# Kernel optimization log

Measured on AMD Instinct MI355X. Metric: run time of the kernel, lower is better.

Reference implementation:

```python
import jax, jax.numpy as jnp
import numpy as np

H, W, R = 512, 512, 4
H8, W8 = H // 8, W // 8  # 64, 64
B, C = 4, 256


def _offsets(r):
    # diamond window: y in [-r, r], x in [|y|-r, r-|y|]  ->  2r^2+2r+1 offsets
    offs = []
    for y in range(-r, r + 1):
        for x in range(abs(y) - r, r - abs(y) + 1):
            offs.append((y, x))
    return np.asarray(offs, dtype=np.float32)  # [L, 2] = (dy, dx)

_OFFS = _offsets(R)  # L = 41


def _corr_pyramid(f1, f2):
    # over the second image's spatial dims for each pyramid level.
    c = jnp.einsum('bcij,bcuv->bijuv', f1, f2) / jnp.sqrt(jnp.float32(f1.shape[1]))
    pyr = [c]
    for _ in range(3):
        b, i, j, h, w = pyr[-1].shape
        pyr.append(pyr[-1].reshape(b, i, j, h // 2, 2, w // 2, 2).mean(axis=(4, 6)))
    return pyr  # shapes [B,64,64,64/2^k,64/2^k] for k=0..3


def _bilinear_zeros(volf, py, px, h, w):
    # volf: [B,H8,W8,h*w]; py/px: [B,H8,W8,L] pixel coords; zero padding.
    y0 = jnp.floor(py); x0 = jnp.floor(px)
    wy1 = py - y0; wy0 = 1.0 - wy1
    wx1 = px - x0; wx0 = 1.0 - wx1

    def gather(yi, xi):
        valid = (yi >= 0) & (yi < h) & (xi >= 0) & (xi < w)
        yc = jnp.clip(yi, 0, h - 1).astype(jnp.int32)
        xc = jnp.clip(xi, 0, w - 1).astype(jnp.int32)
        v = jnp.take_along_axis(volf, yc * w + xc, axis=-1)
        return jnp.where(valid, v, jnp.zeros((), volf.dtype))

    return (wy0 * wx0 * gather(y0, x0) + wy0 * wx1 * gather(y0, x0 + 1)
            + wy1 * wx0 * gather(y0 + 1, x0) + wy1 * wx1 * gather(y0 + 1, x0 + 1))


def _lookup_level(corr, flow, k):
    # corr: [B,H8,W8,h,w]; flow: [B,2,H8,W8] (chan 0 = dy, chan 1 = dx)
    b, _, _, h, w = corr.shape
    dy = jnp.asarray(_OFFS[:, 0]); dx = jnp.asarray(_OFFS[:, 1])
    ii = jnp.arange(H8, dtype=corr.dtype)[:, None]   # [H8,1]
    jj = jnp.arange(W8, dtype=corr.dtype)[None, :]   # [1,W8]
    scale = jnp.float32(2.0 ** k)
    yc = (ii[None] + flow[:, 0]) / scale             # [B,H8,W8]
    xc = (jj[None] + flow[:, 1]) / scale
    py = yc[..., None] + dy                          # [B,H8,W8,L]
    px = xc[..., None] + dx
    # original normalizes by dim/2 (not (dim-1)/2), grid_sample align_corners=True
    # maps normalized g -> pixel (g+1)*(dim-1)/2, net: pixel = coord*(dim-1)/dim
    py = py * (h - 1) / h
    px = px * (w - 1) / w
    volf = corr.reshape(b, H8, W8, h * w)
    return _bilinear_zeros(volf, py, px, h, w)       # [B,H8,W8,L]


def setup_inputs() -> dict:
    key = jax.random.key(0)
    k1, k2, k3 = jax.random.split(key, 3)
    feat1 = jax.random.normal(k1, (B, C, H8, W8), dtype=jnp.float32)
    feat2 = jax.random.normal(k2, (B, C, H8, W8), dtype=jnp.float32)
    curr_flow = jax.random.normal(k3, (B, 2, H8, W8), dtype=jnp.float32)
    return {"feat1": feat1, "feat2": feat2, "curr_flow": curr_flow}


def reference(feat1, feat2, curr_flow):
    pyr = _corr_pyramid(feat1, feat2)
    lookups = [_lookup_level(pyr[k], curr_flow, k) for k in range(4)]
    return jnp.stack(lookups, axis=3)  # [B, H8, W8, 4, 41]
```

## Files before the change

### kernel.cpp

```cpp
#include <hip/hip_runtime.h>
#include <stdint.h>

#define NB 4
#define NC 256
#define FB   1392640
#define LVO1 1048576
#define LVO2 1310720
#define LVO3 1376256

typedef short bf16x8 __attribute__((ext_vector_type(8)));
typedef float f32x4  __attribute__((ext_vector_type(4)));

__device__ __forceinline__ unsigned short f2b(float x){
  uint32_t u = __float_as_uint(x);
  return (unsigned short)((u + 0x7FFFu + ((u >> 16) & 1u)) >> 16);
}
__device__ __forceinline__ unsigned int pack2(float a, float b){
  return (unsigned int)f2b(a) | ((unsigned int)f2b(b) << 16);
}

__global__ __launch_bounds__(256) void prep_all(const float* __restrict__ f1,
                 const float* __restrict__ f2,
                 unsigned short* __restrict__ f1t,
                 unsigned short* __restrict__ f2c){
  __shared__ float lds[128*65];
  __shared__ float l1s[32*65];
  __shared__ float l2s[8*65];
  const int t = threadIdx.x;
  const int bx = blockIdx.x;

  if (bx < 2048){
    const int b = bx >> 9, rest = bx & 511;
    const int cc = rest >> 7, pt = rest & 127;
    const int p0 = pt*32, c0 = cc*64;
    const int tx = t & 31, ty = t >> 5;
    float (*tileF)[33] = (float(*)[33])lds;
    #pragma unroll
    for (int r = 0; r < 8; ++r){
      int c = ty + r*8;
      tileF[c][tx] = f1[((size_t)(b*NC) + c0 + c)*4096 + p0 + tx];
    }
    __syncthreads();
    #pragma unroll
    for (int r = 0; r < 4; ++r){
      int pl = ty + r*8;
      size_t o = ((size_t)(b*4096 + p0 + pl))*NC;
      *(unsigned int*)(f1t + o + c0 + 2*tx) = pack2(tileF[2*tx][pl], tileF[2*tx+1][pl]);
    }
  } else {
    const int fid = bx - 2048;
    const int b = fid >> 7, rest = fid & 127;
    const int reg = rest >> 2, cc = rest & 3;
    const int i0 = (reg >> 2) * 8, j0 = (reg & 3) * 16;
    const int c0 = cc * 64, qb = cc * 8;

    #pragma unroll
    for (int it = 0; it < 8; ++it){
      int q = t + 256*it;
      int ch = q >> 5, rc = q & 31, ri = rc >> 2, c4 = rc & 3;
      const float4 v = *(const float4*)(f2 + ((size_t)(b*NC) + c0 + ch)*4096
                                          + (i0+ri)*64 + j0 + c4*4);
      float* dstL = lds + (ri*16 + c4*4)*65 + ch;
      dstL[0] = v.x; dstL[65] = v.y; dstL[130] = v.z; dstL[195] = v.w;
    }
    __syncthreads();
    unsigned short* f2cB = f2c + (size_t)b*FB;

    #pragma unroll
    for (int it = 0; it < 4; ++it){
      int idx = t + 256*it;
      int cell = idx & 127, qi = idx >> 7;
      int ci = cell >> 4, cj = cell & 15;
      const float* src = lds + cell*65 + qi*8;
      uint4 v;
      v.x = pack2(src[0], src[1]); v.y = pack2(src[2], src[3]);
      v.z = pack2(src[4], src[5]); v.w = pack2(src[6], src[7]);
      int cellg = (i0+ci)*64 + j0+cj;
      *(uint4*)(f2cB + ((size_t)(qb+qi)*4096 + cellg)*8) = v;
    }
    {
      int cell = t & 31, qi = t >> 5;
      int a = cell >> 3, bc = cell & 7;
      const float* p00 = lds + ((2*a)*16 + 2*bc)*65 + qi*8;
      float s[8];
      #pragma unroll
      for (int j = 0; j < 8; ++j){
        s[j] = p00[j] + p00[65+j] + p00[16*65+j] + p00[17*65+j];
        l1s[cell*65 + qi*8 + j] = s[j];
      }
      uint4 v;
      v.x = pack2(s[0]*0.25f, s[1]*0.25f); v.y = pack2(s[2]*0.25f, s[3]*0.25f);
      v.z = pack2(s[4]*0.25f, s[5]*0.25f); v.w = pack2(s[6]*0.25f, s[7]*0.25f);
      int cellg = ((i0>>1)+a)*32 + (j0>>1)+bc;
      *(uint4*)(f2cB + LVO1 + ((size_t)(qb+qi)*1024 + cellg)*8) = v;
    }
    __syncthreads();
    if (t < 64){
      int cell = t & 7, qi = t >> 3;
      int a2 = cell >> 2, bc2 = cell & 3;
      float s[8];
      #pragma unroll
      for (int j = 0; j < 8; ++j){
        int ch = qi*8 + j;
        s[j] = l1s[((2*a2)*8   + 2*bc2  )*65 + ch] + l1s[((2*a2)*8   + 2*bc2+1)*65 + ch]
             + l1s[((2*a2+1)*8 + 2*bc2  )*65 + ch] + l1s[((2*a2+1)*8 + 2*bc2+1)*65 + ch];
        l2s[cell*65 + ch] = s[j];
      }
      uint4 v;
      v.x = pack2(s[0]*0.0625f, s[1]*0.0625f); v.y = pack2(s[2]*0.0625f, s[3]*0.0625f);
      v.z = pack2(s[4]*0.0625f, s[5]*0.0625f); v.w = pack2(s[6]*0.0625f, s[7]*0.0625f);
      int cellg = ((i0>>2)+a2)*16 + (j0>>2)+bc2;
      *(uint4*)(f2cB + LVO2 + ((size_t)(qb+qi)*256 + cellg)*8) = v;
    }
    __syncthreads();
    if (t < 16){
      int cl = t & 1, qi = t >> 1;
      float s[8];
      #pragma unroll
      for (int j = 0; j < 8; ++j){
        int ch = qi*8 + j;
        s[j] = l2s[(0*4 + 2*cl)*65 + ch] + l2s[(0*4 + 2*cl+1)*65 + ch]
             + l2s[(1*4 + 2*cl)*65 + ch] + l2s[(1*4 + 2*cl+1)*65 + ch];
      }
      const float m = 1.0f/64.0f;
      uint4 v;
      v.x = pack2(s[0]*m, s[1]*m); v.y = pack2(s[2]*m, s[3]*m);
      v.z = pack2(s[4]*m, s[5]*m); v.w = pack2(s[6]*m, s[7]*m);
      int cellg = (i0>>3)*8 + (j0>>3) + cl;
      *(uint4*)(f2cB + LVO3 + ((size_t)(qb+qi)*64 + cellg)*8) = v;
    }
  }
}

__global__ __launch_bounds__(256, 4) void lookup_main(const float* __restrict__ flow,
                 const unsigned short* __restrict__ f1t,
                 const unsigned short* __restrict__ f2c,
                 float* __restrict__ out){
  const int lane = threadIdx.x & 63;
  const int wid  = threadIdx.x >> 6;
  const int blk = blockIdx.x;
  const int xs = blk & 7;
  const int bb = xs >> 1;
  const int tile = ((blk >> 3) << 1) | (xs & 1);
  const int ti4 = (tile >> 4) << 2;
  const int tj4 = (tile & 15) << 2;

  __shared__ float box[4*16*113];
  __shared__ int   ls_y0[64], ls_x0[64];
  __shared__ float ls_f[32];
  __shared__ int   ls_meta[32];

  {
    float4* b4 = (float4*)box;
    for (int q = threadIdx.x; q < (4*16*113)/4; q += 256)
      b4[q] = make_float4(0.f, 0.f, 0.f, 0.f);
  }

  const int n = lane & 15;
  const int g = lane >> 4;
  const int pn = ((ti4 + (n >> 2)) << 6) + tj4 + (n & 3);

  bf16x8 bfr[8];
  {
    const unsigned short* f1c = f1t + ((size_t)(bb*4096 + pn))*NC;
    #pragma unroll
    for (int st = 0; st < 8; ++st)
      bfr[st] = *(const bf16x8*)(f1c + st*32 + g*8);
  }

  if (wid == 0){
    const int k = g;
    const int i_n = pn >> 6, j_n = pn & 63;
    const float fy = flow[((bb*2 + 0)*64 + i_n)*64 + j_n];
    const float fx = flow[((bb*2 + 1)*64 + i_n)*64 + j_n];
    if (k == 0){ ls_f[n] = fy; ls_f[16 + n] = fx; }
    const int h = 64 >> k;
    const float inv = 1.0f / (float)(1 << k);
    const float s = (float)(h - 1) / (float)h;
    const float yc = ((float)i_n + fy) * inv;
    const float xc = ((float)j_n + fx) * inv;
    const int y0 = (int)floorf((yc - 4.0f) * s);
    const int x0 = (int)floorf((xc - 4.0f) * s);
    ls_y0[k*16 + n] = y0;
    ls_x0[k*16 + n] = x0;
    int ymin = y0, ymax = y0, xmin = x0, xmax = x0;
    #pragma unroll
    for (int m = 1; m < 16; m <<= 1){
      ymin = min(ymin, __shfl_xor(ymin, m));
      ymax = max(ymax, __shfl_xor(ymax, m));
      xmin = min(xmin, __shfl_xor(xmin, m));
      xmax = max(xmax, __shfl_xor(xmax, m));
    }
    if (n == 0){
      int ylo = max(ymin, 0), yhi = min(ymax + 9, h - 1);
      int xlo = max(xmin, 0), xhi = min(xmax + 9, h - 1);
      int H = max(yhi - ylo + 1, 0), W = max(xhi - xlo + 1, 0);
      int cells = W * H;
      ls_meta[k*8 + 0] = ylo;
      ls_meta[k*8 + 1] = xlo;
      ls_meta[k*8 + 2] = W;
      ls_meta[k*8 + 3] = cells;
      ls_meta[k*8 + 4] = __float_as_int(1.0f / (float)W);
      ls_meta[k*8 + 5] = (k==0) ? 0 : (k==1) ? LVO1 : (k==2) ? LVO2 : LVO3;
      ls_meta[k*8 + 6] = (cells + 15) >> 4;
    }
  }
  __syncthreads();

  const int y0n0 = ls_y0[n],      x0n0 = ls_x0[n];
  const int y0n1 = ls_y0[16 + n], x0n1 = ls_x0[16 + n];
  const int y0n2 = ls_y0[32 + n], x0n2 = ls_x0[32 + n];
  const int y0n3 = ls_y0[48 + n], x0n3 = ls_x0[48 + n];
  const int pre1 = ls_meta[6];
  const int pre2 = pre1 + ls_meta[14];
  const int pre3 = pre2 + ls_meta[22];
  const int P    = pre3 + ls_meta[30];
  const unsigned short* f2cB = f2c + (size_t)bb*FB;

  for (int p = wid; p < P; p += 4){
    const int k  = (p >= pre1) + (p >= pre2) + (p >= pre3);
    const int lp = p - ((k==0) ? 0 : (k==1) ? pre1 : (k==2) ? pre2 : pre3);
    const int mb = k*8;
    const int ylo = ls_meta[mb], xlo = ls_meta[mb+1], W = ls_meta[mb+2];
    const int cells = ls_meta[mb+3];
    const float rW = __int_as_float(ls_meta[mb+4]);
    const int lvoc = ls_meta[mb+5];
    const int h = 64 >> k;
    const int ncl = h*h;
    const int base = lp << 4;

    const int idxA = min(base + n, cells - 1);
    const int by = (int)fmaf((float)idxA, rW, 0.004f);
    const int bx = idxA - by*W;
    const int cellIdx = (ylo + by)*h + (xlo + bx);
    const unsigned short* colp = f2cB + lvoc + ((size_t)(g*ncl + cellIdx) << 3);
    const int strideS = ncl << 5;

    f32x4 acc0 = {0.f,0.f,0.f,0.f}, acc1 = {0.f,0.f,0.f,0.f};
    #pragma unroll
    for (int st = 0; st < 8; st += 2){
      bf16x8 a0 = *(const bf16x8*)(colp + (size_t)st*strideS);
      bf16x8 a1 = *(const bf16x8*)(colp + (size_t)(st+1)*strideS);
      acc0 = __builtin_amdgcn_mfma_f32_16x16x32_bf16(a0, bfr[st],   acc0, 0, 0, 0);
      acc1 = __builtin_amdgcn_mfma_f32_16x16x32_bf16(a1, bfr[st+1], acc1, 0, 0, 0);
    }
    const int yb = (k==0) ? y0n0 : (k==1) ? y0n1 : (k==2) ? y0n2 : y0n3;
    const int xb = (k==0) ? x0n0 : (k==1) ? x0n1 : (k==2) ? x0n2 : x0n3;
    #pragma unroll
    for (int r = 0; r < 4; ++r){
      const int ci = base + (g << 2) + r;
      if (ci < cells){
        const int byc = (int)fmaf((float)ci, rW, 0.004f);
        const int bxc = ci - byc*W;
        const int ry = ylo + byc - yb;
        const int rx = xlo + bxc - xb;
        if ((unsigned)ry < 10u && (unsigned)rx < 10u)
          box[(k*16 + n)*113 + ry*10 + rx] = (acc0[r] + acc1[r]) * 0.0625f;
      }
    }
  }
  __syncthreads();

  int dy = 0, dx = 0;
  {
    int rem = lane;
    #pragma unroll
    for (int ry = -4; ry <= 4; ++ry){
      int ab = ry < 0 ? -ry : ry;
      int ln = 9 - 2*ab;
      if (rem >= 0 && rem < ln){ dy = ry; dx = rem + (ab - 4); }
      rem -= ln;
    }
  }
  const int k = wid;
  const float inv = 1.0f / (float)(1 << k);
  const float s = (float)((64 >> k) - 1) / (float)(64 >> k);
  if (lane < 41){
    for (int t = 0; t < 16; ++t){
      const int pt = ((ti4 + (t >> 2)) << 6) + tj4 + (t & 3);
      const float fy = ls_f[t], fx = ls_f[16 + t];
      const float yc = ((float)(pt >> 6) + fy) * inv;
      const float xc = ((float)(pt & 63) + fx) * inv;
      const float py = (yc + (float)dy) * s;
      const float px = (xc + (float)dx) * s;
      const float fy0 = floorf(py), fx0 = floorf(px);
      const float wy1 = py - fy0, wx1 = px - fx0;
      const float wy0 = 1.0f - wy1, wx0 = 1.0f - wx1;
      const int iy = (int)fy0 - ls_y0[k*16 + t];
      const int ix = (int)fx0 - ls_x0[k*16 + t];
      const float* bx_ = &box[(k*16 + t)*113 + iy*10 + ix];
      const float v = wy0*(wx0*bx_[0] + wx1*bx_[1]) + wy1*(wx0*bx_[10] + wx1*bx_[11]);
      out[((size_t)(bb*4096 + pt)*4 + k)*41 + lane] = v;
    }
  }
}

extern "C" void kernel_launch(void* const* d_in, const int* in_sizes, int n_in,
                              void* d_out, int out_size, void* d_ws, size_t ws_size,
                              hipStream_t stream){
  const float* feat1 = (const float*)d_in[0];
  const float* feat2 = (const float*)d_in[1];
  const float* flow  = (const float*)d_in[2];
  float* out = (float*)d_out;
  unsigned short* f1t = (unsigned short*)d_ws;
  unsigned short* f2c = f1t + (size_t)NB*4096*NC;

  prep_all<<<2560, 256, 0, stream>>>(feat1, feat2, f1t, f2c);
  lookup_main<<<1024, 256, 0, stream>>>(flow, f1t, f2c, out);
}
```

Before: 111.2 us.

## Software-pipeline A-fragment loads in lookup loop and widen feat1 transpose tiles

The lookup loop now prefetches the next work item's eight bf16 A fragments and metadata before running the MFMAs on the current item, so global-load latency overlaps with compute. Separately, the feat1 transpose in the prep kernel uses 64x64 tiles with float4 loads and 16-byte packed bf16 stores, which halves that part of the grid. Double-buffered fragments raise register pressure under launch_bounds(256,4), and the wider tile may bring more LDS bank conflicts on the strided reads.

```diff
diff --git a/kernel.cpp b/kernel.cpp
--- a/kernel.cpp
+++ b/kernel.cpp
@@ -29,26 +29,33 @@
   const int t = threadIdx.x;
   const int bx = blockIdx.x;
 
-  if (bx < 2048){
-    const int b = bx >> 9, rest = bx & 511;
-    const int cc = rest >> 7, pt = rest & 127;
-    const int p0 = pt*32, c0 = cc*64;
-    const int tx = t & 31, ty = t >> 5;
-    float (*tileF)[33] = (float(*)[33])lds;
-    #pragma unroll
-    for (int r = 0; r < 8; ++r){
-      int c = ty + r*8;
-      tileF[c][tx] = f1[((size_t)(b*NC) + c0 + c)*4096 + p0 + tx];
+  if (bx < 1024){
+    const int b = bx >> 8;
+    const int rest = bx & 255;
+    const int pt = rest >> 2, cc = rest & 3;
+    const int p0 = pt*64, c0 = cc*64;
+    #pragma unroll
+    for (int it = 0; it < 4; ++it){
+      int idx = t + 256*it;
+      int row = idx >> 4, c4 = idx & 15;
+      const float4 v = *(const float4*)(f1 + ((size_t)(b*NC) + c0 + row)*4096
+                                          + p0 + c4*4);
+      float* d = lds + row*65 + c4*4;
+      d[0]=v.x; d[1]=v.y; d[2]=v.z; d[3]=v.w;
     }
     __syncthreads();
     #pragma unroll
-    for (int r = 0; r < 4; ++r){
-      int pl = ty + r*8;
-      size_t o = ((size_t)(b*4096 + p0 + pl))*NC;
-      *(unsigned int*)(f1t + o + c0 + 2*tx) = pack2(tileF[2*tx][pl], tileF[2*tx+1][pl]);
+    for (int it = 0; it < 2; ++it){
+      int idx = t + 256*it;
+      int px = idx >> 3, ch8 = idx & 7;
+      const float* s = lds + (ch8*8)*65 + px;
+      uint4 v;
+      v.x = pack2(s[0],   s[65]);  v.y = pack2(s[130], s[195]);
+      v.z = pack2(s[260], s[325]); v.w = pack2(s[390], s[455]);
+      *(uint4*)(f1t + ((size_t)(b*4096 + p0 + px))*NC + c0 + ch8*8) = v;
     }
   } else {
-    const int fid = bx - 2048;
+    const int fid = bx - 1024;
     const int b = fid >> 7, rest = fid & 127;
     const int reg = rest >> 2, cc = rest & 3;
     const int i0 = (reg >> 2) * 8, j0 = (reg & 3) * 16;
@@ -131,6 +138,12 @@
     }
   }
 }
+
+struct PM {
+  const unsigned short* colp;
+  int strideS, k, base, ylo, xlo, W, cells, yb, xb;
+  float rW;
+};
 
 __global__ __launch_bounds__(256, 4) void lookup_main(const float* __restrict__ flow,
                  const unsigned short* __restrict__ f1t,
@@ -217,47 +230,70 @@
   const int P    = pre3 + ls_meta[30];
   const unsigned short* f2cB = f2c + (size_t)bb*FB;
 
-  for (int p = wid; p < P; p += 4){
-    const int k  = (p >= pre1) + (p >= pre2) + (p >= pre3);
-    const int lp = p - ((k==0) ? 0 : (k==1) ? pre1 : (k==2) ? pre2 : pre3);
-    const int mb = k*8;
-    const int ylo = ls_meta[mb], xlo = ls_meta[mb+1], W = ls_meta[mb+2];
-    const int cells = ls_meta[mb+3];
-    const float rW = __int_as_float(ls_meta[mb+4]);
+  auto mk = [&](int p)->PM{
+    PM m;
+    m.k = (p >= pre1) + (p >= pre2) + (p >= pre3);
+    const int lp = p - ((m.k==0) ? 0 : (m.k==1) ? pre1 : (m.k==2) ? pre2 : pre3);
+    const int mb = m.k*8;
+    m.ylo = ls_meta[mb]; m.xlo = ls_meta[mb+1]; m.W = ls_meta[mb+2];
+    m.cells = ls_meta[mb+3]; m.rW = __int_as_float(ls_meta[mb+4]);
     const int lvoc = ls_meta[mb+5];
-    const int h = 64 >> k;
-    const int ncl = h*h;
-    const int base = lp << 4;
-
-    const int idxA = min(base + n, cells - 1);
-    const int by = (int)fmaf((float)idxA, rW, 0.004f);
-    const int bx = idxA - by*W;
-    const int cellIdx = (ylo + by)*h + (xlo + bx);
-    const unsigned short* colp = f2cB + lvoc + ((size_t)(g*ncl + cellIdx) << 3);
-    const int strideS = ncl << 5;
-
+    const int h = 64 >> m.k, ncl = h*h;
+    m.base = lp << 4;
+    const int idxA = min(m.base + n, m.cells - 1);
+    const int by = (int)fmaf((float)idxA, m.rW, 0.004f);
+    const int bx = idxA - by*m.W;
+    m.colp = f2cB + lvoc + ((size_t)(g*ncl + (m.ylo + by)*h + (m.xlo + bx)) << 3);
+    m.strideS = ncl << 5;
+    m.yb = (m.k==0) ? y0n0 : (m.k==1) ? y0n1 : (m.k==2) ? y0n2 : y0n3;
+    m.xb = (m.k==0) ? x0n0 : (m.k==1) ? x0n1 : (m.k==2) ? x0n2 : x0n3;
+    return m;
+  };
+
+  bf16x8 afr[8];
+  PM cur;
+  int p = wid;
+  if (p < P){
+    cur = mk(p);
+    #pragma unroll
+    for (int st = 0; st < 8; ++st)
+      afr[st] = *(const bf16x8*)(cur.colp + (size_t)st*cur.strideS);
+  }
+  while (p < P){
+    const int np = p + 4;
+    PM nxt;
+    bf16x8 nfr[8];
+    const bool has = np < P;
+    if (has){
+      nxt = mk(np);
+      #pragma unroll
+      for (int st = 0; st < 8; ++st)
+        nfr[st] = *(const bf16x8*)(nxt.colp + (size_t)st*nxt.strideS);
+    }
     f32x4 acc0 = {0.f,0.f,0.f,0.f}, acc1 = {0.f,0.f,0.f,0.f};
     #pragma unroll
     for (int st = 0; st < 8; st += 2){
-      bf16x8 a0 = *(const bf16x8*)(colp + (size_t)st*strideS);
-      bf16x8 a1 = *(const bf16x8*)(colp + (size_t)(st+1)*strideS);
-      acc0 = __builtin_amdgcn_mfma_f32_16x16x32_bf16(a0, bfr[st],   acc0, 0, 0, 0);
-      acc1 = __builtin_amdgcn_mfma_f32_16x16x32_bf16(a1, bfr[st+1], acc1, 0, 0, 0);
-    }
-    const int yb = (k==0) ? y0n0 : (k==1) ? y0n1 : (k==2) ? y0n2 : y0n3;
-    const int xb = (k==0) ? x0n0 : (k==1) ? x0n1 : (k==2) ? x0n2 : x0n3;
+      acc0 = __builtin_amdgcn_mfma_f32_16x16x32_bf16(afr[st],   bfr[st],   acc0, 0, 0, 0);
+      acc1 = __builtin_amdgcn_mfma_f32_16x16x32_bf16(afr[st+1], bfr[st+1], acc1, 0, 0, 0);
+    }
     #pragma unroll
     for (int r = 0; r < 4; ++r){
-      const int ci = base + (g << 2) + r;
-      if (ci < cells){
-        const int byc = (int)fmaf((float)ci, rW, 0.004f);
-        const int bxc = ci - byc*W;
-        const int ry = ylo + byc - yb;
-        const int rx = xlo + bxc - xb;
+      const int ci = cur.base + (g << 2) + r;
+      if (ci < cur.cells){
+        const int byc = (int)fmaf((float)ci, cur.rW, 0.004f);
+        const int bxc = ci - byc*cur.W;
+        const int ry = cur.ylo + byc - cur.yb;
+        const int rx = cur.xlo + bxc - cur.xb;
         if ((unsigned)ry < 10u && (unsigned)rx < 10u)
-          box[(k*16 + n)*113 + ry*10 + rx] = (acc0[r] + acc1[r]) * 0.0625f;
+          box[(cur.k*16 + n)*113 + ry*10 + rx] = (acc0[r] + acc1[r]) * 0.0625f;
       }
     }
+    if (has){
+      cur = nxt;
+      #pragma unroll
+      for (int st = 0; st < 8; ++st) afr[st] = nfr[st];
+    }
+    p = np;
   }
   __syncthreads();
 
@@ -305,6 +341,6 @@
   unsigned short* f1t = (unsigned short*)d_ws;
   unsigned short* f2c = f1t + (size_t)NB*4096*NC;
 
-  prep_all<<<2560, 256, 0, stream>>>(feat1, feat2, f1t, f2c);
+  prep_all<<<1536, 256, 0, stream>>>(feat1, feat2, f1t, f2c);
   lookup_main<<<1024, 256, 0, stream>>>(flow, f1t, f2c, out);
 }
```

Measured after the change: 127.0 us. 1.14x slower.

## Fuse feat1 transpose and bf16 conversion into lookup kernel via LDS

Applied to the files above, without the earlier changes.

Removes the feat1 transpose/convert blocks from the prep kernel. The lookup kernel now loads its 16 query pixels' fp32 feat1 channels directly, converts them to bf16 into a padded LDS tile, and reads the MFMA B fragments from LDS. This drops the f1t workspace round-trip (write, then read) and cuts the prep grid from 2560 to 512 blocks. In exchange it adds about 8 KB of LDS per block and strided global reads of feat1 inside lookup_main, which may lower occupancy.

```diff
diff --git a/kernel.cpp b/kernel.cpp
--- a/kernel.cpp
+++ b/kernel.cpp
@@ -19,121 +19,97 @@
   return (unsigned int)f2b(a) | ((unsigned int)f2b(b) << 16);
 }
 
-__global__ __launch_bounds__(256) void prep_all(const float* __restrict__ f1,
-                 const float* __restrict__ f2,
-                 unsigned short* __restrict__ f1t,
+__global__ __launch_bounds__(256) void prep_all(const float* __restrict__ f2,
                  unsigned short* __restrict__ f2c){
   __shared__ float lds[128*65];
   __shared__ float l1s[32*65];
   __shared__ float l2s[8*65];
   const int t = threadIdx.x;
-  const int bx = blockIdx.x;
-
-  if (bx < 2048){
-    const int b = bx >> 9, rest = bx & 511;
-    const int cc = rest >> 7, pt = rest & 127;
-    const int p0 = pt*32, c0 = cc*64;
-    const int tx = t & 31, ty = t >> 5;
-    float (*tileF)[33] = (float(*)[33])lds;
-    #pragma unroll
-    for (int r = 0; r < 8; ++r){
-      int c = ty + r*8;
-      tileF[c][tx] = f1[((size_t)(b*NC) + c0 + c)*4096 + p0 + tx];
-    }
-    __syncthreads();
-    #pragma unroll
-    for (int r = 0; r < 4; ++r){
-      int pl = ty + r*8;
-      size_t o = ((size_t)(b*4096 + p0 + pl))*NC;
-      *(unsigned int*)(f1t + o + c0 + 2*tx) = pack2(tileF[2*tx][pl], tileF[2*tx+1][pl]);
-    }
-  } else {
-    const int fid = bx - 2048;
-    const int b = fid >> 7, rest = fid & 127;
-    const int reg = rest >> 2, cc = rest & 3;
-    const int i0 = (reg >> 2) * 8, j0 = (reg & 3) * 16;
-    const int c0 = cc * 64, qb = cc * 8;
-
-    #pragma unroll
-    for (int it = 0; it < 8; ++it){
-      int q = t + 256*it;
-      int ch = q >> 5, rc = q & 31, ri = rc >> 2, c4 = rc & 3;
-      const float4 v = *(const float4*)(f2 + ((size_t)(b*NC) + c0 + ch)*4096
-                                          + (i0+ri)*64 + j0 + c4*4);
-      float* dstL = lds + (ri*16 + c4*4)*65 + ch;
-      dstL[0] = v.x; dstL[65] = v.y; dstL[130] = v.z; dstL[195] = v.w;
-    }
-    __syncthreads();
-    unsigned short* f2cB = f2c + (size_t)b*FB;
-
-    #pragma unroll
-    for (int it = 0; it < 4; ++it){
-      int idx = t + 256*it;
-      int cell = idx & 127, qi = idx >> 7;
-      int ci = cell >> 4, cj = cell & 15;
-      const float* src = lds + cell*65 + qi*8;
-      uint4 v;
-      v.x = pack2(src[0], src[1]); v.y = pack2(src[2], src[3]);
-      v.z = pack2(src[4], src[5]); v.w = pack2(src[6], src[7]);
-      int cellg = (i0+ci)*64 + j0+cj;
-      *(uint4*)(f2cB + ((size_t)(qb+qi)*4096 + cellg)*8) = v;
-    }
-    {
-      int cell = t & 31, qi = t >> 5;
-      int a = cell >> 3, bc = cell & 7;
-      const float* p00 = lds + ((2*a)*16 + 2*bc)*65 + qi*8;
-      float s[8];
-      #pragma unroll
-      for (int j = 0; j < 8; ++j){
-        s[j] = p00[j] + p00[65+j] + p00[16*65+j] + p00[17*65+j];
-        l1s[cell*65 + qi*8 + j] = s[j];
-      }
-      uint4 v;
-      v.x = pack2(s[0]*0.25f, s[1]*0.25f); v.y = pack2(s[2]*0.25f, s[3]*0.25f);
-      v.z = pack2(s[4]*0.25f, s[5]*0.25f); v.w = pack2(s[6]*0.25f, s[7]*0.25f);
-      int cellg = ((i0>>1)+a)*32 + (j0>>1)+bc;
-      *(uint4*)(f2cB + LVO1 + ((size_t)(qb+qi)*1024 + cellg)*8) = v;
-    }
-    __syncthreads();
-    if (t < 64){
-      int cell = t & 7, qi = t >> 3;
-      int a2 = cell >> 2, bc2 = cell & 3;
-      float s[8];
-      #pragma unroll
-      for (int j = 0; j < 8; ++j){
-        int ch = qi*8 + j;
-        s[j] = l1s[((2*a2)*8   + 2*bc2  )*65 + ch] + l1s[((2*a2)*8   + 2*bc2+1)*65 + ch]
-             + l1s[((2*a2+1)*8 + 2*bc2  )*65 + ch] + l1s[((2*a2+1)*8 + 2*bc2+1)*65 + ch];
-        l2s[cell*65 + ch] = s[j];
-      }
-      uint4 v;
-      v.x = pack2(s[0]*0.0625f, s[1]*0.0625f); v.y = pack2(s[2]*0.0625f, s[3]*0.0625f);
-      v.z = pack2(s[4]*0.0625f, s[5]*0.0625f); v.w = pack2(s[6]*0.0625f, s[7]*0.0625f);
-      int cellg = ((i0>>2)+a2)*16 + (j0>>2)+bc2;
-      *(uint4*)(f2cB + LVO2 + ((size_t)(qb+qi)*256 + cellg)*8) = v;
-    }
-    __syncthreads();
-    if (t < 16){
-      int cl = t & 1, qi = t >> 1;
-      float s[8];
-      #pragma unroll
-      for (int j = 0; j < 8; ++j){
-        int ch = qi*8 + j;
-        s[j] = l2s[(0*4 + 2*cl)*65 + ch] + l2s[(0*4 + 2*cl+1)*65 + ch]
-             + l2s[(1*4 + 2*cl)*65 + ch] + l2s[(1*4 + 2*cl+1)*65 + ch];
-      }
-      const float m = 1.0f/64.0f;
-      uint4 v;
-      v.x = pack2(s[0]*m, s[1]*m); v.y = pack2(s[2]*m, s[3]*m);
-      v.z = pack2(s[4]*m, s[5]*m); v.w = pack2(s[6]*m, s[7]*m);
-      int cellg = (i0>>3)*8 + (j0>>3) + cl;
-      *(uint4*)(f2cB + LVO3 + ((size_t)(qb+qi)*64 + cellg)*8) = v;
-    }
+  const int fid = blockIdx.x;
+  const int b = fid >> 7, rest = fid & 127;
+  const int reg = rest >> 2, cc = rest & 3;
+  const int i0 = (reg >> 2) * 8, j0 = (reg & 3) * 16;
+  const int c0 = cc * 64, qb = cc * 8;
+
+  #pragma unroll
+  for (int it = 0; it < 8; ++it){
+    int q = t + 256*it;
+    int ch = q >> 5, rc = q & 31, ri = rc >> 2, c4 = rc & 3;
+    const float4 v = *(const float4*)(f2 + ((size_t)(b*NC) + c0 + ch)*4096
+                                        + (i0+ri)*64 + j0 + c4*4);
+    float* dstL = lds + (ri*16 + c4*4)*65 + ch;
+    dstL[0] = v.x; dstL[65] = v.y; dstL[130] = v.z; dstL[195] = v.w;
+  }
+  __syncthreads();
+  unsigned short* f2cB = f2c + (size_t)b*FB;
+
+  #pragma unroll
+  for (int it = 0; it < 4; ++it){
+    int idx = t + 256*it;
+    int cell = idx & 127, qi = idx >> 7;
+    int ci = cell >> 4, cj = cell & 15;
+    const float* src = lds + cell*65 + qi*8;
+    uint4 v;
+    v.x = pack2(src[0], src[1]); v.y = pack2(src[2], src[3]);
+    v.z = pack2(src[4], src[5]); v.w = pack2(src[6], src[7]);
+    int cellg = (i0+ci)*64 + j0+cj;
+    *(uint4*)(f2cB + ((size_t)(qb+qi)*4096 + cellg)*8) = v;
+  }
+  {
+    int cell = t & 31, qi = t >> 5;
+    int a = cell >> 3, bc = cell & 7;
+    const float* p00 = lds + ((2*a)*16 + 2*bc)*65 + qi*8;
+    float s[8];
+    #pragma unroll
+    for (int j = 0; j < 8; ++j){
+      s[j] = p00[j] + p00[65+j] + p00[16*65+j] + p00[17*65+j];
+      l1s[cell*65 + qi*8 + j] = s[j];
+    }
+    uint4 v;
+    v.x = pack2(s[0]*0.25f, s[1]*0.25f); v.y = pack2(s[2]*0.25f, s[3]*0.25f);
+    v.z = pack2(s[4]*0.25f, s[5]*0.25f); v.w = pack2(s[6]*0.25f, s[7]*0.25f);
+    int cellg = ((i0>>1)+a)*32 + (j0>>1)+bc;
+    *(uint4*)(f2cB + LVO1 + ((size_t)(qb+qi)*1024 + cellg)*8) = v;
+  }
+  __syncthreads();
+  if (t < 64){
+    int cell = t & 7, qi = t >> 3;
+    int a2 = cell >> 2, bc2 = cell & 3;
+    float s[8];
+    #pragma unroll
+    for (int j = 0; j < 8; ++j){
+      int ch = qi*8 + j;
+      s[j] = l1s[((2*a2)*8   + 2*bc2  )*65 + ch] + l1s[((2*a2)*8   + 2*bc2+1)*65 + ch]
+           + l1s[((2*a2+1)*8 + 2*bc2  )*65 + ch] + l1s[((2*a2+1)*8 + 2*bc2+1)*65 + ch];
+      l2s[cell*65 + ch] = s[j];
+    }
+    uint4 v;
+    v.x = pack2(s[0]*0.0625f, s[1]*0.0625f); v.y = pack2(s[2]*0.0625f, s[3]*0.0625f);
+    v.z = pack2(s[4]*0.0625f, s[5]*0.0625f); v.w = pack2(s[6]*0.0625f, s[7]*0.0625f);
+    int cellg = ((i0>>2)+a2)*16 + (j0>>2)+bc2;
+    *(uint4*)(f2cB + LVO2 + ((size_t)(qb+qi)*256 + cellg)*8) = v;
+  }
+  __syncthreads();
+  if (t < 16){
+    int cl = t & 1, qi = t >> 1;
+    float s[8];
+    #pragma unroll
+    for (int j = 0; j < 8; ++j){
+      int ch = qi*8 + j;
+      s[j] = l2s[(0*4 + 2*cl)*65 + ch] + l2s[(0*4 + 2*cl+1)*65 + ch]
+           + l2s[(1*4 + 2*cl)*65 + ch] + l2s[(1*4 + 2*cl+1)*65 + ch];
+    }
+    const float m = 1.0f/64.0f;
+    uint4 v;
+    v.x = pack2(s[0]*m, s[1]*m); v.y = pack2(s[2]*m, s[3]*m);
+    v.z = pack2(s[4]*m, s[5]*m); v.w = pack2(s[6]*m, s[7]*m);
+    int cellg = (i0>>3)*8 + (j0>>3) + cl;
+    *(uint4*)(f2cB + LVO3 + ((size_t)(qb+qi)*64 + cellg)*8) = v;
   }
 }
 
 __global__ __launch_bounds__(256, 4) void lookup_main(const float* __restrict__ flow,
-                 const unsigned short* __restrict__ f1t,
+                 const float* __restrict__ f1,
                  const unsigned short* __restrict__ f2c,
                  float* __restrict__ out){
   const int lane = threadIdx.x & 63;
@@ -146,6 +122,7 @@
   const int tj4 = (tile & 15) << 2;
 
   __shared__ float box[4*16*113];
+  __shared__ unsigned short f1s[16*264];
   __shared__ int   ls_y0[64], ls_x0[64];
   __shared__ float ls_f[32];
   __shared__ int   ls_meta[32];
@@ -156,17 +133,22 @@
       b4[q] = make_float4(0.f, 0.f, 0.f, 0.f);
   }
 
+  {
+    const float* f1b = f1 + ((size_t)(bb*NC) + threadIdx.x)*4096;
+    #pragma unroll
+    for (int r = 0; r < 4; ++r){
+      const float4 v = *(const float4*)(f1b + (ti4 + r)*64 + tj4);
+      const int px = r*4;
+      f1s[(px+0)*264 + threadIdx.x] = f2b(v.x);
+      f1s[(px+1)*264 + threadIdx.x] = f2b(v.y);
+      f1s[(px+2)*264 + threadIdx.x] = f2b(v.z);
+      f1s[(px+3)*264 + threadIdx.x] = f2b(v.w);
+    }
+  }
+
   const int n = lane & 15;
   const int g = lane >> 4;
   const int pn = ((ti4 + (n >> 2)) << 6) + tj4 + (n & 3);
-
-  bf16x8 bfr[8];
-  {
-    const unsigned short* f1c = f1t + ((size_t)(bb*4096 + pn))*NC;
-    #pragma unroll
-    for (int st = 0; st < 8; ++st)
-      bfr[st] = *(const bf16x8*)(f1c + st*32 + g*8);
-  }
 
   if (wid == 0){
     const int k = g;
@@ -206,6 +188,11 @@
     }
   }
   __syncthreads();
+
+  bf16x8 bfr[8];
+  #pragma unroll
+  for (int st = 0; st < 8; ++st)
+    bfr[st] = *(const bf16x8*)(&f1s[n*264 + st*32 + g*8]);
 
   const int y0n0 = ls_y0[n],      x0n0 = ls_x0[n];
   const int y0n1 = ls_y0[16 + n], x0n1 = ls_x0[16 + n];
@@ -302,9 +289,8 @@
   const float* feat2 = (const float*)d_in[1];
   const float* flow  = (const float*)d_in[2];
   float* out = (float*)d_out;
-  unsigned short* f1t = (unsigned short*)d_ws;
-  unsigned short* f2c = f1t + (size_t)NB*4096*NC;
-
-  prep_all<<<2560, 256, 0, stream>>>(feat1, feat2, f1t, f2c);
-  lookup_main<<<1024, 256, 0, stream>>>(flow, f1t, f2c, out);
-}
+  unsigned short* f2c = (unsigned short*)d_ws;
+
+  prep_all<<<512, 256, 0, stream>>>(feat2, f2c);
+  lookup_main<<<1024, 256, 0, stream>>>(flow, feat1, f2c, out);
+}
```

Measured after the change: 107.5 us (median of 2 runs). -3.3%, faster.
